# Optimization experiments

Hardware: AMD Instinct MI355X
Metric: run time of the kernel (lower is better)

The kernel has to match this reference:

```python
import jax, jax.numpy as jnp
import numpy as np
from jax import lax

IN_CH = 256
FILTERS_PER_CH = 2            # expansion = 1 -> 2 filters per input channel
INTER_CH = IN_CH * FILTERS_PER_CH
BUTTERFLY_SIZE = 8
BUTTERFLIES = INTER_CH // 2 // BUTTERFLY_SIZE  # 32
WING = BUTTERFLY_SIZE // 2                      # 4


def setup_inputs() -> dict:
    key = jax.random.key(0)
    k1, k2 = jax.random.split(key)
    x = jax.random.normal(k1, (32, IN_CH, 56, 56), dtype=jnp.float32)
    # depthwise conv weight, PyTorch OIHW with groups=IN_CH: (INTER_CH, 1, 3, 3)
    w = jax.random.normal(k2, (INTER_CH, 1, 3, 3), dtype=jnp.float32) * 0.1
    return {"x": x, "w": w}


def reference(x, w):
    # grouped (depthwise, channel multiplier 2) conv, stride 1, pad 1, no bias
    y = lax.conv_general_dilated(
        x, w,
        window_strides=(1, 1),
        padding=[(1, 1), (1, 1)],
        feature_group_count=IN_CH,
        dimension_numbers=("NCHW", "OIHW", "NCHW"),
    )  # (B, INTER_CH, H, W); channels group-major: 2i,2i+1 from input i
    B, C2, H, W = y.shape
    # extract_sequences: consecutive channels alternate between the two outputs
    y = y.reshape(B, C2 // 2, 2, H, W)
    x1 = y[:, :, 0]  # (B, IN_CH, H, W)
    x2 = y[:, :, 1]
    # swap_wings: within each butterfly, swap the two wings
    s = x2.reshape(B, BUTTERFLIES, 2, WING, H, W)
    x2 = jnp.flip(s, axis=2).reshape(B, C2 // 2, H, W)
    return x1 + x2
```

## Files before the change

kernel.cpp:

```cpp
#include <hip/hip_runtime.h>

#define IN_CH 256
#define IMG_H 56
#define IMG_W 56
#define QW (IMG_W / 4)

__global__ __launch_bounds__(256) void dwconv_butterfly(
    const float* __restrict__ x, const float* __restrict__ wgt,
    float* __restrict__ out)
{
    const int p  = blockIdx.x;
    const int b  = blockIdx.y;
    const int c0 = ((p >> 2) << 3) | (p & 3);
    const int c1 = c0 ^ 4;

    const size_t chan_elems = (size_t)IMG_H * IMG_W;
    const float* x0 = x + ((size_t)b * IN_CH + c0) * chan_elems;
    const float* x1 = x + ((size_t)b * IN_CH + c1) * chan_elems;
    float* o0 = out + ((size_t)b * IN_CH + c0) * chan_elems;
    float* o1 = out + ((size_t)b * IN_CH + c1) * chan_elems;

    float wa[9], wb[9], wc[9], wd[9];
    {
        const float* pa = wgt + (size_t)(2 * c0) * 9;
        const float* pb = wgt + (size_t)(2 * c1 + 1) * 9;
        const float* pc = wgt + (size_t)(2 * c1) * 9;
        const float* pd = wgt + (size_t)(2 * c0 + 1) * 9;
#pragma unroll
        for (int i = 0; i < 9; ++i) {
            wa[i] = pa[i]; wb[i] = pb[i]; wc[i] = pc[i]; wd[i] = pd[i];
        }
    }

    for (int idx = threadIdx.x; idx < IMG_H * QW; idx += 256) {
        const int h  = idx / QW;
        const int j  = idx - h * QW;
        const int w0 = j * 4;

        float acc0[4] = {0.f, 0.f, 0.f, 0.f};
        float acc1[4] = {0.f, 0.f, 0.f, 0.f};

#pragma unroll
        for (int kh = 0; kh < 3; ++kh) {
            const int hh = h + kh - 1;
            float r0[6], r1[6];
            if (hh >= 0 && hh < IMG_H) {
                const float* row0 = x0 + hh * IMG_W + w0;
                const float* row1 = x1 + hh * IMG_W + w0;
                const float4 v0 = *(const float4*)row0;
                const float4 v1 = *(const float4*)row1;
                r0[1] = v0.x; r0[2] = v0.y; r0[3] = v0.z; r0[4] = v0.w;
                r1[1] = v1.x; r1[2] = v1.y; r1[3] = v1.z; r1[4] = v1.w;
                r0[0] = (w0 > 0)          ? row0[-1] : 0.f;
                r1[0] = (w0 > 0)          ? row1[-1] : 0.f;
                r0[5] = (w0 + 4 < IMG_W)  ? row0[4]  : 0.f;
                r1[5] = (w0 + 4 < IMG_W)  ? row1[4]  : 0.f;
            } else {
#pragma unroll
                for (int i = 0; i < 6; ++i) { r0[i] = 0.f; r1[i] = 0.f; }
            }
#pragma unroll
            for (int kw = 0; kw < 3; ++kw) {
                const float fa = wa[kh * 3 + kw], fb = wb[kh * 3 + kw];
                const float fc = wc[kh * 3 + kw], fd = wd[kh * 3 + kw];
#pragma unroll
                for (int i = 0; i < 4; ++i) {
                    acc0[i] += r0[i + kw] * fa + r1[i + kw] * fb;
                    acc1[i] += r1[i + kw] * fc + r0[i + kw] * fd;
                }
            }
        }

        float4 s0 = make_float4(acc0[0], acc0[1], acc0[2], acc0[3]);
        float4 s1 = make_float4(acc1[0], acc1[1], acc1[2], acc1[3]);
        *(float4*)(o0 + h * IMG_W + w0) = s0;
        *(float4*)(o1 + h * IMG_W + w0) = s1;
    }
}

extern "C" void kernel_launch(void* const* d_in, const int* in_sizes, int n_in,
                              void* d_out, int out_size, void* d_ws, size_t ws_size,
                              hipStream_t stream) {
    const float* x = (const float*)d_in[0];
    const float* w = (const float*)d_in[1];
    float* out = (float*)d_out;

    dim3 grid(IN_CH / 2, 32);
    dim3 block(256);
    dwconv_butterfly<<<grid, block, 0, stream>>>(x, w, out);
}
```

Before: 212.6 us.

## Stage both input channels in padded LDS tiles before the depthwise conv

Each block now loads the full pair of 56x56 input channels into a zero-padded 58x60 LDS buffer using coalesced float4 loads issued up front, then runs the 3x3 stencil from LDS with no boundary branches. This replaces the repeated global loads per output quad (three rows plus unaligned halo elements) with a single global read per element. The per-thread loop is also fully unrolled into fixed iterations. In exchange the kernel uses about 28 KB of LDS per block, which may limit occupancy, and adds a barrier plus LDS access that can bank-conflict on the unaligned float2 reads.

```diff
diff --git a/kernel.cpp b/kernel.cpp
--- a/kernel.cpp
+++ b/kernel.cpp
@@ -3,22 +3,71 @@
 #define IN_CH 256
 #define IMG_H 56
 #define IMG_W 56
-#define QW (IMG_W / 4)
+#define LDS_W 60
+#define LDS_H 58
+#define CH_ELEMS (LDS_W * LDS_H)
 
 __global__ __launch_bounds__(256) void dwconv_butterfly(
     const float* __restrict__ x, const float* __restrict__ wgt,
     float* __restrict__ out)
 {
-    const int p  = blockIdx.x;
-    const int b  = blockIdx.y;
-    const int c0 = ((p >> 2) << 3) | (p & 3);
-    const int c1 = c0 ^ 4;
+    __shared__ float lds[2 * CH_ELEMS];
 
-    const size_t chan_elems = (size_t)IMG_H * IMG_W;
-    const float* x0 = x + ((size_t)b * IN_CH + c0) * chan_elems;
-    const float* x1 = x + ((size_t)b * IN_CH + c1) * chan_elems;
-    float* o0 = out + ((size_t)b * IN_CH + c0) * chan_elems;
-    float* o1 = out + ((size_t)b * IN_CH + c1) * chan_elems;
+    const int tid = threadIdx.x;
+    const int p   = blockIdx.x;
+    const int b   = blockIdx.y;
+    const int c0  = ((p >> 2) << 3) | (p & 3);
+    const int c1  = c0 ^ 4;
+
+    const size_t chan = (size_t)IMG_H * IMG_W;
+    const float* x0 = x + ((size_t)b * IN_CH + c0) * chan;
+    const float* x1 = x + ((size_t)b * IN_CH + c1) * chan;
+    float* o0 = out + ((size_t)b * IN_CH + c0) * chan;
+    float* o1 = out + ((size_t)b * IN_CH + c1) * chan;
+
+    float4 v[6];
+    int    ofs[6];
+#pragma unroll
+    for (int k = 0; k < 6; ++k) {
+        const int q    = tid + 256 * k;
+        const int ch   = (q >= 784) ? 1 : 0;
+        const int rem  = q - ch * 784;
+        const int row  = rem / 14;
+        const int colq = rem - row * 14;
+        const float* src = (ch ? x1 : x0) + row * IMG_W + colq * 4;
+        v[k]   = *(const float4*)src;
+        ofs[k] = ch * CH_ELEMS + (row + 1) * LDS_W + colq * 4 + 1;
+    }
+    float4 v6; int ofs6 = 0; bool has6 = (tid < 32);
+    if (has6) {
+        const int q    = tid + 1536;
+        const int rem  = q - 784;
+        const int row  = rem / 14;
+        const int colq = rem - row * 14;
+        v6   = *(const float4*)(x1 + row * IMG_W + colq * 4);
+        ofs6 = CH_ELEMS + (row + 1) * LDS_W + colq * 4 + 1;
+    }
+
+    for (int i = tid; i < 456; i += 256) {
+        const int ch = i / 228;
+        const int r  = i - ch * 228;
+        int row, col;
+        if (r < 116) { row = (r / 58) * 57; col = r % 58; }
+        else         { const int rr = r - 116; row = 1 + (rr >> 1); col = (rr & 1) * 57; }
+        lds[ch * CH_ELEMS + row * LDS_W + col] = 0.f;
+    }
+
+#pragma unroll
+    for (int k = 0; k < 6; ++k) {
+        float* d = &lds[ofs[k]];
+        d[0] = v[k].x; d[1] = v[k].y; d[2] = v[k].z; d[3] = v[k].w;
+    }
+    if (has6) {
+        float* d = &lds[ofs6];
+        d[0] = v6.x; d[1] = v6.y; d[2] = v6.z; d[3] = v6.w;
+    }
+
+    __syncthreads();
 
     float wa[9], wb[9], wc[9], wd[9];
     {
@@ -32,33 +81,21 @@
         }
     }
 
-    for (int idx = threadIdx.x; idx < IMG_H * QW; idx += 256) {
-        const int h  = idx / QW;
-        const int j  = idx - h * QW;
-        const int w0 = j * 4;
-
+    auto compute_quad = [&](int idx) {
+        const int h  = idx / 14;
+        const int w0 = (idx - h * 14) * 4;
         float acc0[4] = {0.f, 0.f, 0.f, 0.f};
         float acc1[4] = {0.f, 0.f, 0.f, 0.f};
-
 #pragma unroll
         for (int kh = 0; kh < 3; ++kh) {
-            const int hh = h + kh - 1;
-            float r0[6], r1[6];
-            if (hh >= 0 && hh < IMG_H) {
-                const float* row0 = x0 + hh * IMG_W + w0;
-                const float* row1 = x1 + hh * IMG_W + w0;
-                const float4 v0 = *(const float4*)row0;
-                const float4 v1 = *(const float4*)row1;
-                r0[1] = v0.x; r0[2] = v0.y; r0[3] = v0.z; r0[4] = v0.w;
-                r1[1] = v1.x; r1[2] = v1.y; r1[3] = v1.z; r1[4] = v1.w;
-                r0[0] = (w0 > 0)          ? row0[-1] : 0.f;
-                r1[0] = (w0 > 0)          ? row1[-1] : 0.f;
-                r0[5] = (w0 + 4 < IMG_W)  ? row0[4]  : 0.f;
-                r1[5] = (w0 + 4 < IMG_W)  ? row1[4]  : 0.f;
-            } else {
-#pragma unroll
-                for (int i = 0; i < 6; ++i) { r0[i] = 0.f; r1[i] = 0.f; }
-            }
+            const float* p0 = &lds[(h + kh) * LDS_W + w0];
+            const float* p1 = p0 + CH_ELEMS;
+            const float4 a0 = *(const float4*)p0;
+            const float2 b0 = *(const float2*)(p0 + 4);
+            const float4 a1 = *(const float4*)p1;
+            const float2 b1 = *(const float2*)(p1 + 4);
+            const float r0[6] = {a0.x, a0.y, a0.z, a0.w, b0.x, b0.y};
+            const float r1[6] = {a1.x, a1.y, a1.z, a1.w, b1.x, b1.y};
 #pragma unroll
             for (int kw = 0; kw < 3; ++kw) {
                 const float fa = wa[kh * 3 + kw], fb = wb[kh * 3 + kw];
@@ -70,12 +107,13 @@
                 }
             }
         }
+        *(float4*)(o0 + h * IMG_W + w0) = make_float4(acc0[0], acc0[1], acc0[2], acc0[3]);
+        *(float4*)(o1 + h * IMG_W + w0) = make_float4(acc1[0], acc1[1], acc1[2], acc1[3]);
+    };
 
-        float4 s0 = make_float4(acc0[0], acc0[1], acc0[2], acc0[3]);
-        float4 s1 = make_float4(acc1[0], acc1[1], acc1[2], acc1[3]);
-        *(float4*)(o0 + h * IMG_W + w0) = s0;
-        *(float4*)(o1 + h * IMG_W + w0) = s1;
-    }
+#pragma unroll
+    for (int k = 0; k < 3; ++k) compute_quad(tid + 256 * k);
+    if (tid < 16) compute_quad(768 + tid);
 }
 
 extern "C" void kernel_launch(void* const* d_in, const int* in_sizes, int n_in,
```

Result: faster. 182.2 us (-14.3%).

## Register-tile 4x4 output per thread with shuffle-based halo and nontemporal stores

Applied to the files above, without the earlier changes.

Each thread now computes a 4-row by 4-column output tile, loading 6 input rows once into registers so vertical halo rows are reused across the 4 outputs instead of reloaded. Horizontal halo elements come from neighbouring lanes via warp shuffles rather than extra scalar global loads. Outputs are written with nontemporal stores to avoid polluting cache. The fixed 16x16 thread mapping leaves some threads idle and raises register pressure.

```diff
diff --git a/kernel.cpp b/kernel.cpp
--- a/kernel.cpp
+++ b/kernel.cpp
@@ -3,22 +3,28 @@
 #define IN_CH 256
 #define IMG_H 56
 #define IMG_W 56
-#define QW (IMG_W / 4)
+
+typedef float v4f __attribute__((ext_vector_type(4)));
 
 __global__ __launch_bounds__(256) void dwconv_butterfly(
     const float* __restrict__ x, const float* __restrict__ wgt,
     float* __restrict__ out)
 {
+    const int tid = threadIdx.x;
+    const int s   = tid >> 4;
+    const int i   = tid & 15;
+    const bool active = (s < 14) && (i < 14);
+
     const int p  = blockIdx.x;
     const int b  = blockIdx.y;
     const int c0 = ((p >> 2) << 3) | (p & 3);
     const int c1 = c0 ^ 4;
 
-    const size_t chan_elems = (size_t)IMG_H * IMG_W;
-    const float* x0 = x + ((size_t)b * IN_CH + c0) * chan_elems;
-    const float* x1 = x + ((size_t)b * IN_CH + c1) * chan_elems;
-    float* o0 = out + ((size_t)b * IN_CH + c0) * chan_elems;
-    float* o1 = out + ((size_t)b * IN_CH + c1) * chan_elems;
+    const size_t chan = (size_t)IMG_H * IMG_W;
+    const float* x0 = x + ((size_t)b * IN_CH + c0) * chan;
+    const float* x1 = x + ((size_t)b * IN_CH + c1) * chan;
+    float* o0 = out + ((size_t)b * IN_CH + c0) * chan;
+    float* o1 = out + ((size_t)b * IN_CH + c1) * chan;
 
     float wa[9], wb[9], wc[9], wd[9];
     {
@@ -27,54 +33,68 @@
         const float* pc = wgt + (size_t)(2 * c1) * 9;
         const float* pd = wgt + (size_t)(2 * c0 + 1) * 9;
 #pragma unroll
-        for (int i = 0; i < 9; ++i) {
-            wa[i] = pa[i]; wb[i] = pb[i]; wc[i] = pc[i]; wd[i] = pd[i];
+        for (int k = 0; k < 9; ++k) {
+            wa[k] = pa[k]; wb[k] = pb[k]; wc[k] = pc[k]; wd[k] = pd[k];
         }
     }
 
-    for (int idx = threadIdx.x; idx < IMG_H * QW; idx += 256) {
-        const int h  = idx / QW;
-        const int j  = idx - h * QW;
-        const int w0 = j * 4;
+    const int row0 = 4 * s - 1;
+    const int col  = 4 * i;
 
+    float4 v0[6], v1[6];
+#pragma unroll
+    for (int k = 0; k < 6; ++k) {
+        const int  rr = row0 + k;
+        const bool ok = active && (rr >= 0) && (rr < IMG_H);
+        if (ok) {
+            v0[k] = *(const float4*)(x0 + rr * IMG_W + col);
+            v1[k] = *(const float4*)(x1 + rr * IMG_W + col);
+        } else {
+            v0[k] = make_float4(0.f, 0.f, 0.f, 0.f);
+            v1[k] = make_float4(0.f, 0.f, 0.f, 0.f);
+        }
+    }
+
+    float l0[6], r0h[6], l1[6], r1h[6];
+#pragma unroll
+    for (int k = 0; k < 6; ++k) {
+        const float a = __shfl_up(v0[k].w, 1);
+        const float bb = __shfl_up(v1[k].w, 1);
+        const float c = __shfl_down(v0[k].x, 1);
+        const float d = __shfl_down(v1[k].x, 1);
+        l0[k]  = (i == 0)  ? 0.f : a;
+        l1[k]  = (i == 0)  ? 0.f : bb;
+        r0h[k] = (i == 13) ? 0.f : c;
+        r1h[k] = (i == 13) ? 0.f : d;
+    }
+
+#pragma unroll
+    for (int m = 0; m < 4; ++m) {
         float acc0[4] = {0.f, 0.f, 0.f, 0.f};
         float acc1[4] = {0.f, 0.f, 0.f, 0.f};
-
 #pragma unroll
         for (int kh = 0; kh < 3; ++kh) {
-            const int hh = h + kh - 1;
-            float r0[6], r1[6];
-            if (hh >= 0 && hh < IMG_H) {
-                const float* row0 = x0 + hh * IMG_W + w0;
-                const float* row1 = x1 + hh * IMG_W + w0;
-                const float4 v0 = *(const float4*)row0;
-                const float4 v1 = *(const float4*)row1;
-                r0[1] = v0.x; r0[2] = v0.y; r0[3] = v0.z; r0[4] = v0.w;
-                r1[1] = v1.x; r1[2] = v1.y; r1[3] = v1.z; r1[4] = v1.w;
-                r0[0] = (w0 > 0)          ? row0[-1] : 0.f;
-                r1[0] = (w0 > 0)          ? row1[-1] : 0.f;
-                r0[5] = (w0 + 4 < IMG_W)  ? row0[4]  : 0.f;
-                r1[5] = (w0 + 4 < IMG_W)  ? row1[4]  : 0.f;
-            } else {
-#pragma unroll
-                for (int i = 0; i < 6; ++i) { r0[i] = 0.f; r1[i] = 0.f; }
-            }
+            const int k = m + kh;
+            const float e0[6] = {l0[k], v0[k].x, v0[k].y, v0[k].z, v0[k].w, r0h[k]};
+            const float e1[6] = {l1[k], v1[k].x, v1[k].y, v1[k].z, v1[k].w, r1h[k]};
 #pragma unroll
             for (int kw = 0; kw < 3; ++kw) {
                 const float fa = wa[kh * 3 + kw], fb = wb[kh * 3 + kw];
                 const float fc = wc[kh * 3 + kw], fd = wd[kh * 3 + kw];
 #pragma unroll
-                for (int i = 0; i < 4; ++i) {
-                    acc0[i] += r0[i + kw] * fa + r1[i + kw] * fb;
-                    acc1[i] += r1[i + kw] * fc + r0[i + kw] * fd;
+                for (int q = 0; q < 4; ++q) {
+                    acc0[q] += e0[q + kw] * fa + e1[q + kw] * fb;
+                    acc1[q] += e1[q + kw] * fc + e0[q + kw] * fd;
                 }
             }
         }
-
-        float4 s0 = make_float4(acc0[0], acc0[1], acc0[2], acc0[3]);
-        float4 s1 = make_float4(acc1[0], acc1[1], acc1[2], acc1[3]);
-        *(float4*)(o0 + h * IMG_W + w0) = s0;
-        *(float4*)(o1 + h * IMG_W + w0) = s1;
+        if (active) {
+            const int orow = 4 * s + m;
+            v4f s0 = {acc0[0], acc0[1], acc0[2], acc0[3]};
+            v4f s1 = {acc1[0], acc1[1], acc1[2], acc1[3]};
+            __builtin_nontemporal_store(s0, (v4f*)(o0 + orow * IMG_W + col));
+            __builtin_nontemporal_store(s1, (v4f*)(o1 + orow * IMG_W + col));
+        }
     }
 }
 
```

After: 190.4 us. 1.12x faster.
